# Performance work log

Hardware: AMD Instinct MI355X
Metric: run time of the kernel (lower is better)

The kernel has to match this reference:

```python
import jax, jax.numpy as jnp
import numpy as np

N_NODES = 100000
N_EDGES = 3200000
D_IN, D_HID, D_OUT = 512, 256, 64


def setup_inputs() -> dict:
    key = jax.random.key(0)
    ks = jax.random.split(key, 8)
    x = jax.random.normal(ks[0], (N_NODES, D_IN), dtype=jnp.float32)
    row = jax.random.randint(ks[1], (N_EDGES,), 0, N_NODES, dtype=jnp.int64)
    col = jax.random.randint(ks[2], (N_EDGES,), 0, N_NODES, dtype=jnp.int64)
    edge_weight = jax.random.uniform(ks[3], (N_EDGES,), dtype=jnp.float32)
    w1 = jax.random.normal(ks[4], (D_IN, D_HID), dtype=jnp.float32) * (1.0 / np.sqrt(D_HID))
    b1 = jax.random.normal(ks[5], (D_HID,), dtype=jnp.float32) * (1.0 / np.sqrt(D_HID))
    w2 = jax.random.normal(ks[6], (D_HID, D_OUT), dtype=jnp.float32) * (1.0 / np.sqrt(D_OUT))
    b2 = jax.random.normal(ks[7], (D_OUT,), dtype=jnp.float32) * (1.0 / np.sqrt(D_OUT))
    return {"x": x, "row": row, "col": col, "edge_weight": edge_weight,
            "w1": w1, "b1": b1, "w2": w2, "b2": b2}


def _gc_layer(h, row, col, edge_weight, w, b, n_nodes):
    # support = h @ w ; out = spmm(adj, support) + b
    support = h @ w                                   # [N, d_out]
    msgs = edge_weight[:, None] * support[col]        # gather source rows
    agg = jax.ops.segment_sum(msgs, row, num_segments=n_nodes)
    return agg + b


def reference(x, row, col, edge_weight, w1, b1, w2, b2):
    n = x.shape[0]
    h = jax.nn.relu(_gc_layer(x, row, col, edge_weight, w1, b1, n))
    # dropout p=0.0 -> identity
    h = _gc_layer(h, row, col, edge_weight, w2, b2, n)
    return jax.nn.log_softmax(h, axis=1)
```

## Files before the change

kernel.cpp:

```cpp
#include <hip/hip_runtime.h>
#include <hip/hip_bf16.h>
#include <hip/hip_fp8.h>

#define N_NODES 100000
#define N_EDGES 3200000
#define D_IN 512
#define D_HID 256
#define D_OUT 64
#define M_PAD 100096

#define NB 782
#define EPB 8192
#define NBLK_BIN ((N_EDGES + EPB - 1) / EPB)

typedef __attribute__((ext_vector_type(8))) short bf16x8;
typedef __attribute__((ext_vector_type(4))) float f32x4;

__device__ __forceinline__ unsigned short f2bf(float f) {
    __hip_bfloat16 h = __float2bfloat16(f);
    return *reinterpret_cast<unsigned short*>(&h);
}
__device__ __forceinline__ float f8f(unsigned int byte) {
    __hip_fp8_e4m3 t;
    t.__x = (__hip_fp8_storage_t)byte;
    return (float)t;
}


__global__ void cast_w1t_kernel(const float* __restrict__ w1, __hip_bfloat16* __restrict__ w1t) {
    int i = blockIdx.x * 256 + threadIdx.x;
    if (i >= D_IN * D_HID) return;
    int k = i / D_HID, n = i % D_HID;
    w1t[n * D_IN + k] = __float2bfloat16(w1[i]);
}

__global__ void cast_w2t_kernel(const float* __restrict__ w2, __hip_bfloat16* __restrict__ w2t) {
    int i = blockIdx.x * 256 + threadIdx.x;
    if (i >= D_HID * D_OUT) return;
    int k = i / D_OUT, n = i % D_OUT;
    w2t[n * D_HID + k] = __float2bfloat16(w2[i]);
}


__global__ __launch_bounds__(256) void hist_bucket_kernel(const int* __restrict__ row,
                                                          int* __restrict__ gcnt) {
    __shared__ int cnt[NB];
    for (int i = threadIdx.x; i < NB; i += 256) cnt[i] = 0;
    __syncthreads();
    int base = blockIdx.x * EPB;
    for (int i = threadIdx.x; i < EPB; i += 256) {
        int e = base + i;
        if (e < N_EDGES) atomicAdd(&cnt[row[e] >> 7], 1);
    }
    __syncthreads();
    for (int i = threadIdx.x; i < NB; i += 256) {
        int c = cnt[i];
        if (c) atomicAdd(&gcnt[i], c);
    }
}

__global__ void scan_nb_kernel(const int* __restrict__ gcnt, int* __restrict__ boff,
                               int* __restrict__ gcur, int* __restrict__ offsets) {
    __shared__ int smem[1024];
    int t = threadIdx.x;
    int v = (t < NB) ? gcnt[t] : 0;
    smem[t] = v;
    __syncthreads();
    for (int off = 1; off < 1024; off <<= 1) {
        int u = (t >= off) ? smem[t - off] : 0;
        __syncthreads();
        smem[t] += u;
        __syncthreads();
    }
    int excl = smem[t] - v;
    if (t < NB) { boff[t] = excl; gcur[t] = excl; }
    if (t == 1023) boff[NB] = smem[1023];
    if (t == 0) offsets[N_NODES] = N_EDGES;
}

__global__ __launch_bounds__(256) void bin_kernel(const int* __restrict__ row,
                                                  const int* __restrict__ col,
                                                  const float* __restrict__ ew,
                                                  int* __restrict__ gcur,
                                                  int2* __restrict__ bucketed) {
    __shared__ int cnt[NB];
    __shared__ int cur[NB];
    for (int i = threadIdx.x; i < NB; i += 256) cnt[i] = 0;
    __syncthreads();
    int base = blockIdx.x * EPB;
    for (int i = threadIdx.x; i < EPB; i += 256) {
        int e = base + i;
        if (e < N_EDGES) atomicAdd(&cnt[row[e] >> 7], 1);
    }
    __syncthreads();
    for (int i = threadIdx.x; i < NB; i += 256) {
        int c = cnt[i];
        cur[i] = c ? atomicAdd(&gcur[i], c) : 0;
    }
    __syncthreads();
    for (int i = threadIdx.x; i < EPB; i += 256) {
        int e = base + i;
        if (e < N_EDGES) {
            int r = row[e];
            int b = r >> 7;
            int pos = atomicAdd(&cur[b], 1);
            bucketed[pos] = make_int2((col[e] << 7) | (r & 127), __float_as_int(ew[e]));
        }
    }
}

__global__ __launch_bounds__(256) void csr_kernel(const int2* __restrict__ bucketed,
                                                  const int* __restrict__ boff,
                                                  int* __restrict__ offsets,
                                                  int2* __restrict__ edges) {
    __shared__ int rcnt[128];
    __shared__ int sc[128];
    __shared__ int rcur[128];
    int b = blockIdx.x;
    int t = threadIdx.x;
    int s = boff[b], e2 = boff[b + 1];
    if (t < 128) rcnt[t] = 0;
    __syncthreads();
    for (int i = s + t; i < e2; i += 256) atomicAdd(&rcnt[bucketed[i].x & 127], 1);
    __syncthreads();
    if (t < 128) sc[t] = rcnt[t];
    __syncthreads();
    for (int off = 1; off < 128; off <<= 1) {
        int u = 0;
        if (t < 128 && t >= off) u = sc[t - off];
        __syncthreads();
        if (t < 128) sc[t] += u;
        __syncthreads();
    }
    if (t < 128) {
        int excl = sc[t] - rcnt[t];
        rcur[t] = excl;
        int rglob = b * 128 + t;
        if (rglob < N_NODES) offsets[rglob] = s + excl;
    }
    __syncthreads();
    for (int i = s + t; i < e2; i += 256) {
        int2 p = bucketed[i];
        int r = p.x & 127;
        int pos = atomicAdd(&rcur[r], 1);
        edges[s + pos] = make_int2(p.x >> 7, p.y);
    }
}


template <int BN, int WROWS, int WCOLS, int MT, int NT, bool A_F32, int OUT_MODE>
__global__ __launch_bounds__(256) void gemm_bf16_kernel(
    const void* __restrict__ Av, const __hip_bfloat16* __restrict__ Bt,
    void* __restrict__ Cv, int K, int Mvalid, int Nld) {
    constexpr int BM = 128;
    constexpr int BK = 32;
    constexpr int LDT = BK + 8;
    __shared__ __align__(16) __hip_bfloat16 As[BM][LDT];
    __shared__ __align__(16) __hip_bfloat16 Bs[BN][LDT];

    const int tid = threadIdx.x;
    const int m0 = blockIdx.x * BM;
    const int n0 = blockIdx.y * BN;
    const int w = tid >> 6, lane = tid & 63;
    const int wr = w % WROWS, wc = w / WROWS;
    const int mbase = wr * MT * 16, nbase = wc * NT * 16;
    const int quad = lane >> 4, l16 = lane & 15;

    f32x4 acc[MT][NT] = {};

    constexpr int ACH = (BM * BK) / (256 * 8);
    constexpr int BCH = (BN * BK) / (256 * 8);

    for (int k0 = 0; k0 < K; k0 += BK) {
#pragma unroll
        for (int c = 0; c < ACH; ++c) {
            int idx = (tid + c * 256) * 8;
            int r = idx / BK, kk = idx % BK;
            if constexpr (A_F32) {
                int grow = m0 + r;
                uint4 o;
                if (grow < Mvalid) {
                    const float* ap = (const float*)Av + (size_t)grow * K + k0 + kk;
                    float4 f0 = *reinterpret_cast<const float4*>(ap);
                    float4 f1 = *reinterpret_cast<const float4*>(ap + 4);
                    o.x = (unsigned)f2bf(f0.x) | ((unsigned)f2bf(f0.y) << 16);
                    o.y = (unsigned)f2bf(f0.z) | ((unsigned)f2bf(f0.w) << 16);
                    o.z = (unsigned)f2bf(f1.x) | ((unsigned)f2bf(f1.y) << 16);
                    o.w = (unsigned)f2bf(f1.z) | ((unsigned)f2bf(f1.w) << 16);
                } else {
                    o = uint4{0, 0, 0, 0};
                }
                *reinterpret_cast<uint4*>(&As[r][kk]) = o;
            } else {
                *reinterpret_cast<uint4*>(&As[r][kk]) = *reinterpret_cast<const uint4*>(
                    (const __hip_bfloat16*)Av + (size_t)(m0 + r) * K + k0 + kk);
            }
        }
#pragma unroll
        for (int c = 0; c < BCH; ++c) {
            int idx = (tid + c * 256) * 8;
            int r = idx / BK, kk = idx % BK;
            *reinterpret_cast<uint4*>(&Bs[r][kk]) =
                *reinterpret_cast<const uint4*>(&Bt[(size_t)(n0 + r) * K + k0 + kk]);
        }
        __syncthreads();

        bf16x8 af[MT], bfr[NT];
#pragma unroll
        for (int mt = 0; mt < MT; ++mt)
            af[mt] = *reinterpret_cast<bf16x8*>(&As[mbase + mt * 16 + l16][quad * 8]);
#pragma unroll
        for (int nt = 0; nt < NT; ++nt)
            bfr[nt] = *reinterpret_cast<bf16x8*>(&Bs[nbase + nt * 16 + l16][quad * 8]);
#pragma unroll
        for (int mt = 0; mt < MT; ++mt)
#pragma unroll
            for (int nt = 0; nt < NT; ++nt)
                acc[mt][nt] = __builtin_amdgcn_mfma_f32_16x16x32_bf16(af[mt], bfr[nt],
                                                                      acc[mt][nt], 0, 0, 0);
        __syncthreads();
    }

#pragma unroll
    for (int mt = 0; mt < MT; ++mt)
#pragma unroll
        for (int nt = 0; nt < NT; ++nt)
#pragma unroll
            for (int r = 0; r < 4; ++r) {
                int rowi = m0 + mbase + mt * 16 + quad * 4 + r;
                int coli = n0 + nbase + nt * 16 + l16;
                if (rowi < Mvalid) {
                    if constexpr (OUT_MODE == 0) {
                        ((float*)Cv)[(size_t)rowi * Nld + coli] = acc[mt][nt][r];
                    } else if constexpr (OUT_MODE == 1) {
                        ((__hip_bfloat16*)Cv)[(size_t)rowi * Nld + coli] =
                            __float2bfloat16(acc[mt][nt][r]);
                    } else {
                        __hip_fp8_e4m3 q(acc[mt][nt][r]);
                        ((unsigned char*)Cv)[(size_t)rowi * Nld + coli] = q.__x;
                    }
                }
            }
}


__global__ __launch_bounds__(256) void agg1_kernel(
    const unsigned int* __restrict__ sup,
    const int* __restrict__ offsets, const int2* __restrict__ edges,
    const float* __restrict__ b1, __hip_bfloat16* __restrict__ hb) {
    int n = blockIdx.x * 4 + (threadIdx.x >> 6);
    int lane = threadIdx.x & 63;
    if (n >= M_PAD) return;
    if (n >= N_NODES) {
        *reinterpret_cast<ushort4*>(&hb[(size_t)n * D_HID + lane * 4]) = ushort4{0, 0, 0, 0};
        return;
    }
    int s = offsets[n], e2 = offsets[n + 1];
    float a0 = 0.f, a1 = 0.f, a2 = 0.f, a3 = 0.f;
    int e = s;
    for (; e + 8 <= e2; e += 8) {
        int2 m[8];
        unsigned int v[8];
#pragma unroll
        for (int i = 0; i < 8; ++i) m[i] = edges[e + i];
#pragma unroll
        for (int i = 0; i < 8; ++i) v[i] = sup[(size_t)m[i].x * 64 + lane];
#pragma unroll
        for (int i = 0; i < 8; ++i) {
            float wv = __int_as_float(m[i].y);
            a0 += wv * f8f(v[i] & 0xff);
            a1 += wv * f8f((v[i] >> 8) & 0xff);
            a2 += wv * f8f((v[i] >> 16) & 0xff);
            a3 += wv * f8f(v[i] >> 24);
        }
    }
    for (; e < e2; ++e) {
        int2 m = edges[e];
        unsigned int v = sup[(size_t)m.x * 64 + lane];
        float wv = __int_as_float(m.y);
        a0 += wv * f8f(v & 0xff);
        a1 += wv * f8f((v >> 8) & 0xff);
        a2 += wv * f8f((v >> 16) & 0xff);
        a3 += wv * f8f(v >> 24);
    }
    float4 bb = reinterpret_cast<const float4*>(b1)[lane];
    ushort4 o;
    o.x = f2bf(fmaxf(a0 + bb.x, 0.f));
    o.y = f2bf(fmaxf(a1 + bb.y, 0.f));
    o.z = f2bf(fmaxf(a2 + bb.z, 0.f));
    o.w = f2bf(fmaxf(a3 + bb.w, 0.f));
    *reinterpret_cast<ushort4*>(&hb[(size_t)n * D_HID + lane * 4]) = o;
}

__global__ __launch_bounds__(256) void agg2_softmax_kernel(
    const unsigned short* __restrict__ sup2, const int* __restrict__ offsets,
    const int2* __restrict__ edges, const float* __restrict__ b2, float* __restrict__ out) {
    int n = blockIdx.x * 4 + (threadIdx.x >> 6);
    int j = threadIdx.x & 63;
    if (n >= N_NODES) return;
    int s = offsets[n], e2 = offsets[n + 1];
    float acc = 0.f;
    int e = s;
    for (; e + 4 <= e2; e += 4) {
        int2 m0 = edges[e], m1 = edges[e + 1], m2 = edges[e + 2], m3 = edges[e + 3];
        float v0 = __uint_as_float((unsigned)sup2[(size_t)m0.x * D_OUT + j] << 16);
        float v1 = __uint_as_float((unsigned)sup2[(size_t)m1.x * D_OUT + j] << 16);
        float v2 = __uint_as_float((unsigned)sup2[(size_t)m2.x * D_OUT + j] << 16);
        float v3 = __uint_as_float((unsigned)sup2[(size_t)m3.x * D_OUT + j] << 16);
        acc += __int_as_float(m0.y) * v0;
        acc += __int_as_float(m1.y) * v1;
        acc += __int_as_float(m2.y) * v2;
        acc += __int_as_float(m3.y) * v3;
    }
    for (; e < e2; ++e) {
        int2 m = edges[e];
        acc += __int_as_float(m.y) * __uint_as_float((unsigned)sup2[(size_t)m.x * D_OUT + j] << 16);
    }
    acc += b2[j];
    float m = acc;
#pragma unroll
    for (int o = 32; o > 0; o >>= 1) m = fmaxf(m, __shfl_xor(m, o, 64));
    float ex = __expf(acc - m);
    float ssum = ex;
#pragma unroll
    for (int o = 32; o > 0; o >>= 1) ssum += __shfl_xor(ssum, o, 64);
    out[(size_t)n * D_OUT + j] = acc - m - __logf(ssum);
}


extern "C" void kernel_launch(void* const* d_in, const int* in_sizes, int n_in,
                              void* d_out, int out_size, void* d_ws, size_t ws_size,
                              hipStream_t stream) {
    const float* x  = (const float*)d_in[0];
    const int* row  = (const int*)d_in[1];
    const int* col  = (const int*)d_in[2];
    const float* ew = (const float*)d_in[3];
    const float* w1 = (const float*)d_in[4];
    const float* b1 = (const float*)d_in[5];
    const float* w2 = (const float*)d_in[6];
    const float* b2 = (const float*)d_in[7];
    float* out = (float*)d_out;

    char* ws = (char*)d_ws;
    size_t off = 0;
    auto alloc = [&](size_t bytes) -> void* {
        void* p = ws + off;
        off = (off + bytes + 255) & ~(size_t)255;
        return p;
    };

    __hip_bfloat16* w1t  = (__hip_bfloat16*)alloc((size_t)D_HID * D_IN * 2);
    __hip_bfloat16* w2t  = (__hip_bfloat16*)alloc((size_t)D_OUT * D_HID * 2);
    unsigned char* sup1  = (unsigned char*)alloc((size_t)N_NODES * D_HID);
    __hip_bfloat16* hb   = (__hip_bfloat16*)alloc((size_t)M_PAD * D_HID * 2);
    unsigned short* sup2 = (unsigned short*)alloc((size_t)N_NODES * D_OUT * 2);
    int* offsets         = (int*)alloc((size_t)(N_NODES + 1) * 4);
    int* gcnt            = (int*)alloc((size_t)NB * 4);
    int* boff            = (int*)alloc((size_t)(NB + 1) * 4);
    int* gcur            = (int*)alloc((size_t)NB * 4);
    int2* edges          = (int2*)alloc((size_t)N_EDGES * 8);
    int2* bucketed       = (int2*)alloc((size_t)N_EDGES * 8);

    hipMemsetAsync(gcnt, 0, (size_t)NB * 4, stream);
    hist_bucket_kernel<<<NBLK_BIN, 256, 0, stream>>>(row, gcnt);
    scan_nb_kernel<<<1, 1024, 0, stream>>>(gcnt, boff, gcur, offsets);
    bin_kernel<<<NBLK_BIN, 256, 0, stream>>>(row, col, ew, gcur, bucketed);
    csr_kernel<<<NB, 256, 0, stream>>>(bucketed, boff, offsets, edges);

    cast_w1t_kernel<<<(D_IN * D_HID + 255) / 256, 256, 0, stream>>>(w1, w1t);
    cast_w2t_kernel<<<(D_HID * D_OUT + 255) / 256, 256, 0, stream>>>(w2, w2t);

    gemm_bf16_kernel<128, 2, 2, 4, 4, true, 2><<<dim3(M_PAD / 128, D_HID / 128), 256, 0, stream>>>(
        x, w1t, sup1, D_IN, N_NODES, D_HID);
    agg1_kernel<<<M_PAD / 4, 256, 0, stream>>>((const unsigned int*)sup1, offsets, edges, b1, hb);

    gemm_bf16_kernel<64, 4, 1, 2, 4, false, 1><<<dim3(M_PAD / 128, 1), 256, 0, stream>>>(
        hb, w2t, sup2, D_HID, N_NODES, D_OUT);
    agg2_softmax_kernel<<<(N_NODES + 3) / 4, 256, 0, stream>>>(sup2, offsets, edges, b2, out);
}
```

Before: 766.7 us.

## Load GEMM tiles directly into LDS via global_load_lds with XOR swizzle

Replaces register-staged global-to-LDS tile loads in the bf16 GEMM with direct global_load_lds 16-byte transfers. The first GEMM now keeps fp32 x in LDS and converts to bf16 when fragments are read. An XOR swizzle replaces the padded layout to avoid bank conflicts. This removes VGPR staging and conversion on the load path, at the cost of doubled LDS for the fp32 A tile, conversion work repeated per wave that reads each row, and rows past Mload left unwritten in LDS.

```diff
diff --git a/kernel.cpp b/kernel.cpp
--- a/kernel.cpp
+++ b/kernel.cpp
@@ -24,6 +24,12 @@
     __hip_fp8_e4m3 t;
     t.__x = (__hip_fp8_storage_t)byte;
     return (float)t;
+}
+
+__device__ __forceinline__ void gload_lds16(const void* g, void* l) {
+    __builtin_amdgcn_global_load_lds(
+        (const __attribute__((address_space(1))) unsigned int*)g,
+        (__attribute__((address_space(3))) unsigned int*)l, 16, 0, 0);
 }
 
 
@@ -151,12 +157,13 @@
 template <int BN, int WROWS, int WCOLS, int MT, int NT, bool A_F32, int OUT_MODE>
 __global__ __launch_bounds__(256) void gemm_bf16_kernel(
     const void* __restrict__ Av, const __hip_bfloat16* __restrict__ Bt,
-    void* __restrict__ Cv, int K, int Mvalid, int Nld) {
+    void* __restrict__ Cv, int K, int Mvalid, int Mload, int Nld) {
     constexpr int BM = 128;
     constexpr int BK = 32;
-    constexpr int LDT = BK + 8;
-    __shared__ __align__(16) __hip_bfloat16 As[BM][LDT];
-    __shared__ __align__(16) __hip_bfloat16 Bs[BN][LDT];
+    constexpr int ABYTES = BM * BK * (A_F32 ? 4 : 2);
+    constexpr int BBYTES = BN * BK * 2;
+    __shared__ __align__(16) unsigned char As[ABYTES];
+    __shared__ __align__(16) unsigned char Bs[BBYTES];
 
     const int tid = threadIdx.x;
     const int m0 = blockIdx.x * BM;
@@ -168,50 +175,64 @@
 
     f32x4 acc[MT][NT] = {};
 
-    constexpr int ACH = (BM * BK) / (256 * 8);
-    constexpr int BCH = (BN * BK) / (256 * 8);
+    constexpr int AISS = ABYTES / (256 * 16);
+    constexpr int BISS = BBYTES / (256 * 16);
 
     for (int k0 = 0; k0 < K; k0 += BK) {
 #pragma unroll
-        for (int c = 0; c < ACH; ++c) {
-            int idx = (tid + c * 256) * 8;
-            int r = idx / BK, kk = idx % BK;
+        for (int c = 0; c < AISS; ++c) {
+            int idx = c * 256 + tid;
             if constexpr (A_F32) {
-                int grow = m0 + r;
-                uint4 o;
-                if (grow < Mvalid) {
-                    const float* ap = (const float*)Av + (size_t)grow * K + k0 + kk;
-                    float4 f0 = *reinterpret_cast<const float4*>(ap);
-                    float4 f1 = *reinterpret_cast<const float4*>(ap + 4);
-                    o.x = (unsigned)f2bf(f0.x) | ((unsigned)f2bf(f0.y) << 16);
-                    o.y = (unsigned)f2bf(f0.z) | ((unsigned)f2bf(f0.w) << 16);
-                    o.z = (unsigned)f2bf(f1.x) | ((unsigned)f2bf(f1.y) << 16);
-                    o.w = (unsigned)f2bf(f1.z) | ((unsigned)f2bf(f1.w) << 16);
-                } else {
-                    o = uint4{0, 0, 0, 0};
+                int r = idx >> 3, slot = idx & 7;
+                if (m0 + r < Mload) {
+                    const float* src = (const float*)Av + (size_t)(m0 + r) * K + k0 +
+                                       ((slot ^ (r & 7)) << 2);
+                    gload_lds16(src, As + idx * 16);
                 }
-                *reinterpret_cast<uint4*>(&As[r][kk]) = o;
             } else {
-                *reinterpret_cast<uint4*>(&As[r][kk]) = *reinterpret_cast<const uint4*>(
-                    (const __hip_bfloat16*)Av + (size_t)(m0 + r) * K + k0 + kk);
+                int r = idx >> 2, slot = idx & 3;
+                if (m0 + r < Mload) {
+                    const __hip_bfloat16* src = (const __hip_bfloat16*)Av +
+                                                (size_t)(m0 + r) * K + k0 +
+                                                ((slot ^ (r & 3)) << 3);
+                    gload_lds16(src, As + idx * 16);
+                }
             }
         }
 #pragma unroll
-        for (int c = 0; c < BCH; ++c) {
-            int idx = (tid + c * 256) * 8;
-            int r = idx / BK, kk = idx % BK;
-            *reinterpret_cast<uint4*>(&Bs[r][kk]) =
-                *reinterpret_cast<const uint4*>(&Bt[(size_t)(n0 + r) * K + k0 + kk]);
+        for (int c = 0; c < BISS; ++c) {
+            int idx = c * 256 + tid;
+            int r = idx >> 2, slot = idx & 3;
+            const __hip_bfloat16* src = Bt + (size_t)(n0 + r) * K + k0 +
+                                        ((slot ^ (r & 3)) << 3);
+            gload_lds16(src, Bs + idx * 16);
         }
         __syncthreads();
 
         bf16x8 af[MT], bfr[NT];
 #pragma unroll
-        for (int mt = 0; mt < MT; ++mt)
-            af[mt] = *reinterpret_cast<bf16x8*>(&As[mbase + mt * 16 + l16][quad * 8]);
-#pragma unroll
-        for (int nt = 0; nt < NT; ++nt)
-            bfr[nt] = *reinterpret_cast<bf16x8*>(&Bs[nbase + nt * 16 + l16][quad * 8]);
+        for (int mt = 0; mt < MT; ++mt) {
+            int r = mbase + mt * 16 + l16;
+            if constexpr (A_F32) {
+                const float4* rowp = (const float4*)(As + r * 128);
+                int sw = r & 7;
+                float4 f0 = rowp[(quad * 2) ^ sw];
+                float4 f1 = rowp[(quad * 2 + 1) ^ sw];
+                union { bf16x8 v; unsigned short u[8]; } o;
+                o.u[0] = f2bf(f0.x); o.u[1] = f2bf(f0.y);
+                o.u[2] = f2bf(f0.z); o.u[3] = f2bf(f0.w);
+                o.u[4] = f2bf(f1.x); o.u[5] = f2bf(f1.y);
+                o.u[6] = f2bf(f1.z); o.u[7] = f2bf(f1.w);
+                af[mt] = o.v;
+            } else {
+                af[mt] = *(const bf16x8*)(As + r * 64 + ((quad ^ (r & 3)) * 16));
+            }
+        }
+#pragma unroll
+        for (int nt = 0; nt < NT; ++nt) {
+            int r = nbase + nt * 16 + l16;
+            bfr[nt] = *(const bf16x8*)(Bs + r * 64 + ((quad ^ (r & 3)) * 16));
+        }
 #pragma unroll
         for (int mt = 0; mt < MT; ++mt)
 #pragma unroll
@@ -371,10 +392,10 @@
     cast_w2t_kernel<<<(D_HID * D_OUT + 255) / 256, 256, 0, stream>>>(w2, w2t);
 
     gemm_bf16_kernel<128, 2, 2, 4, 4, true, 2><<<dim3(M_PAD / 128, D_HID / 128), 256, 0, stream>>>(
-        x, w1t, sup1, D_IN, N_NODES, D_HID);
+        x, w1t, sup1, D_IN, N_NODES, N_NODES, D_HID);
     agg1_kernel<<<M_PAD / 4, 256, 0, stream>>>((const unsigned int*)sup1, offsets, edges, b1, hb);
 
     gemm_bf16_kernel<64, 4, 1, 2, 4, false, 1><<<dim3(M_PAD / 128, 1), 256, 0, stream>>>(
-        hb, w2t, sup2, D_HID, N_NODES, D_OUT);
+        hb, w2t, sup2, D_HID, N_NODES, M_PAD, D_OUT);
     agg2_softmax_kernel<<<(N_NODES + 3) / 4, 256, 0, stream>>>(sup2, offsets, edges, b2, out);
 }
```

Measured after the change: 754.4 us. Within noise of the previous version (-1.6%).
